# Performance work log

Hardware: AMD Instinct MI355X
Metric: run time of the kernel (lower is better)

Reference implementation:

```python
import jax, jax.numpy as jnp
import numpy as np

N_USERS, N_ITEMS, EMB_DIM = 100000, 50000, 64
NNZ = 4800000
N_LAYERS = 3
KEEP_PROB = 0.5
N_NODES = N_USERS + N_ITEMS


def setup_inputs() -> dict:
    key = jax.random.key(0)
    k0, k1, k2, k3, k4, k5 = jax.random.split(key, 6)
    # Xavier-uniform-like init for embedding tables
    bound = float(np.sqrt(6.0 / (N_USERS + EMB_DIM)))
    user_w = jax.random.uniform(k0, (N_USERS, EMB_DIM), jnp.float32, -bound, bound)
    bound_i = float(np.sqrt(6.0 / (N_ITEMS + EMB_DIM)))
    item_w = jax.random.uniform(k1, (N_ITEMS, EMB_DIM), jnp.float32, -bound_i, bound_i)
    # coalesced sparse norm_adj as an edge list; values ~ symmetric-normalized weights
    rows = jax.random.randint(k2, (NNZ,), 0, N_NODES, jnp.int32)
    cols = jax.random.randint(k3, (NNZ,), 0, N_NODES, jnp.int32)
    vals = jax.random.uniform(k4, (NNZ,), jnp.float32) / 32.0
    # sparse-dropout keep mask (rand + keep_prob, floored -> Bernoulli(keep_prob))
    mask = jax.random.bernoulli(k5, KEEP_PROB, (NNZ,))
    return {"user_w": user_w, "item_w": item_w, "vals": vals,
            "rows": rows, "cols": cols, "mask": mask}


def reference(user_w, item_w, vals, rows, cols, mask):
    # sparse dropout: dropped edges contribute 0 to SpMM; kept ones scaled 1/keep_prob
    v = jnp.where(mask, vals / KEEP_PROB, jnp.zeros((), vals.dtype))
    emb = jnp.concatenate([user_w, item_w], axis=0)  # [N, D]
    acc = emb  # running sum over layer outputs (== stack+mean)
    for _ in range(N_LAYERS):
        # SpMM: out[r] += v_e * emb[c] for each edge e=(r,c)
        emb = jax.ops.segment_sum(v[:, None] * emb[cols], rows,
                                  num_segments=N_NODES)
        acc = acc + emb
    out = acc / (N_LAYERS + 1)
    return out[:N_USERS], out[N_USERS:]
```

## Files before the change

### kernel.cpp

```cpp
#include <hip/hip_runtime.h>
#include <hip/hip_fp16.h>

#define DIM 64
#define KEEP_INV 2.0f
#define BROWS 256
#define NB_MAX 640
#define CAP 5120
#define CHUNK 4096
#define SC_T 512
#define EPT 8
#define COLMASK 0x3FFFF

__global__ void init_kernel(const float4* __restrict__ uw,
                            const float4* __restrict__ iw,
                            uint2* __restrict__ embT0,
                            int n_user_v, int total_v,
                            const unsigned char* __restrict__ mask,
                            int* __restrict__ flag,
                            int* __restrict__ gbcur, int nb) {
    if (blockIdx.x == gridDim.x - 1) {
        __shared__ int cnt;
        if (threadIdx.x == 0) cnt = 0;
        __syncthreads();
        int c = 0;
        for (int i = threadIdx.x; i < 4096; i += blockDim.x)
            c += (mask[i] != 0) ? 1 : 0;
        atomicAdd(&cnt, c);
        __syncthreads();
        if (threadIdx.x == 0) *flag = (cnt * 16 > 4096 * 5) ? 1 : 4;
        for (int i = threadIdx.x; i < nb; i += blockDim.x)
            gbcur[i] = i * CAP;
        return;
    }
    int i = blockIdx.x * blockDim.x + threadIdx.x;
    int gs = (gridDim.x - 1) * blockDim.x;
    for (; i < total_v; i += gs) {
        float4 v = (i < n_user_v) ? uw[i] : iw[i - n_user_v];
        __half2 h0 = __float22half2_rn(make_float2(v.x, v.y));
        __half2 h1 = __float22half2_rn(make_float2(v.z, v.w));
        uint2 pk;
        pk.x = *(unsigned int*)&h0;
        pk.y = *(unsigned int*)&h1;
        embT0[i] = pk;
    }
}

__device__ inline int load_keep8(const unsigned char* mask, int e0, int sm) {
    int keep = 0;
    if (sm == 1) {
        uint2 mv = *(const uint2*)(mask + e0);
#pragma unroll
        for (int j = 0; j < 4; ++j) {
            if ((mv.x >> (8 * j)) & 0xFF) keep |= 1 << j;
            if ((mv.y >> (8 * j)) & 0xFF) keep |= 1 << (4 + j);
        }
    } else {
        const int4* mp = (const int4*)((const int*)mask + e0);
        int4 m0 = mp[0], m1 = mp[1];
        if (m0.x) keep |= 1;  if (m0.y) keep |= 2;
        if (m0.z) keep |= 4;  if (m0.w) keep |= 8;
        if (m1.x) keep |= 16; if (m1.y) keep |= 32;
        if (m1.z) keep |= 64; if (m1.w) keep |= 128;
    }
    return keep;
}

__global__ void __launch_bounds__(SC_T, 8) bucket_scatter_kernel(
        const int* __restrict__ rows, const int* __restrict__ cols,
        const float* __restrict__ vals, const unsigned char* __restrict__ mask,
        const int* __restrict__ flag, int nnz, int nb,
        int* __restrict__ gbcur, int2* __restrict__ X) {
    __shared__ int lhist[NB_MAX];
    __shared__ int lcur[NB_MAX];
    int t = threadIdx.x;
    for (int i = t; i < nb; i += SC_T) lhist[i] = 0;
    __syncthreads();
    int sm = *flag;
    int e0 = blockIdx.x * CHUNK + t * EPT;

    int r[EPT], c[EPT];
    float v[EPT];
    int keep = 0;
    if (e0 + EPT <= nnz) {
        const int4* rp = (const int4*)(rows + e0);
        int4 a0 = rp[0], a1 = rp[1];
        r[0] = a0.x; r[1] = a0.y; r[2] = a0.z; r[3] = a0.w;
        r[4] = a1.x; r[5] = a1.y; r[6] = a1.z; r[7] = a1.w;
        const int4* cp = (const int4*)(cols + e0);
        int4 b0 = cp[0], b1 = cp[1];
        c[0] = b0.x; c[1] = b0.y; c[2] = b0.z; c[3] = b0.w;
        c[4] = b1.x; c[5] = b1.y; c[6] = b1.z; c[7] = b1.w;
        const float4* vp = (const float4*)(vals + e0);
        float4 f0 = vp[0], f1 = vp[1];
        v[0] = f0.x; v[1] = f0.y; v[2] = f0.z; v[3] = f0.w;
        v[4] = f1.x; v[5] = f1.y; v[6] = f1.z; v[7] = f1.w;
        keep = load_keep8(mask, e0, sm);
    } else {
        for (int j = 0; j < EPT; ++j) {
            int idx = e0 + j;
            if (idx < nnz) {
                r[j] = rows[idx];
                c[j] = cols[idx];
                v[j] = vals[idx];
                if (mask[(size_t)idx * sm]) keep |= 1 << j;
            }
        }
    }

#pragma unroll
    for (int j = 0; j < EPT; ++j)
        if ((keep >> j) & 1) atomicAdd(&lhist[r[j] >> 8], 1);
    __syncthreads();
    for (int i = t; i < nb; i += SC_T) {
        int cc = lhist[i];
        lcur[i] = cc ? atomicAdd(&gbcur[i], cc) : 0;
    }
    __syncthreads();
#pragma unroll
    for (int j = 0; j < EPT; ++j) {
        if ((keep >> j) & 1) {
            int b = r[j] >> 8;
            int p = atomicAdd(&lcur[b], 1);
            if (p < (b + 1) * CAP) {
                int2 e;
                e.x = (c[j] & COLMASK) | ((r[j] & 255) << 18);
                e.y = __float_as_int(v[j] * KEEP_INV);
                X[p] = e;
            }
        }
    }
}

__global__ void __launch_bounds__(256) bucket_sort_kernel(
        const int2* __restrict__ X, const int* __restrict__ gbcur, int n_nodes,
        int2* __restrict__ Y, int2* __restrict__ rowse) {
    __shared__ int cnt[BROWS];
    __shared__ int sc[2][BROWS];
    __shared__ int rcur[BROWS];
    int b = blockIdx.x;
    int t = threadIdx.x;
    int s0 = b * CAP;
    int count = min(gbcur[b] - s0, CAP);
    int s1 = s0 + count;
    cnt[t] = 0;
    __syncthreads();
    for (int i = s0 + t; i < s1; i += 256) atomicAdd(&cnt[X[i].x >> 18], 1);
    __syncthreads();
    sc[0][t] = cnt[t];
    __syncthreads();
    int src = 0;
    for (int off = 1; off < BROWS; off <<= 1) {
        sc[src ^ 1][t] = sc[src][t] + ((t >= off) ? sc[src][t - off] : 0);
        __syncthreads();
        src ^= 1;
    }
    int excl = (t == 0) ? 0 : sc[src][t - 1];
    rcur[t] = excl;
    int gr = b * BROWS + t;
    if (gr < n_nodes) {
        int2 se;
        se.x = s0 + excl;
        se.y = s0 + excl + cnt[t];
        rowse[gr] = se;
    }
    __syncthreads();
    for (int i = s0 + t; i < s1; i += 256) {
        int2 e = X[i];
        int ro = e.x >> 18;
        int p = atomicAdd(&rcur[ro], 1);
        int2 o;
        o.x = e.x & COLMASK;
        o.y = e.y;
        Y[s0 + p] = o;
    }
}

template <bool STORE_EMB, bool FINAL>
__global__ void __launch_bounds__(256) spmm_kernel(
        const int2* __restrict__ rowse,
        const int2* __restrict__ edges,
        const uint2* __restrict__ embv16,
        uint2* __restrict__ embB16,
        const uint2* __restrict__ e0tab,
        const uint2* __restrict__ e1tab,
        float4* __restrict__ out,
        int nrows) {
    int wid = blockIdx.x * (blockDim.x >> 6) + (threadIdx.x >> 6);
    if (wid >= nrows) return;
    int lane = threadIdx.x & 63;
    int grp = lane >> 4;
    int l16 = lane & 15;
    int2 se = rowse[wid];
    int start = se.x;
    int end = se.y;

    float4 acc;
    acc.x = acc.y = acc.z = acc.w = 0.f;

    for (int e0 = start; e0 < end; e0 += 16) {
        int c[4];
        float v[4];
#pragma unroll
        for (int k = 0; k < 4; ++k) {
            int idx = e0 + grp + 4 * k;
            int cl = idx < end ? idx : end - 1;
            int2 p = edges[cl];
            c[k] = p.x;
            v[k] = (idx < end) ? __int_as_float(p.y) : 0.f;
        }
        uint2 g[4];
#pragma unroll
        for (int k = 0; k < 4; ++k)
            g[k] = embv16[(size_t)c[k] * 16 + l16];
#pragma unroll
        for (int k = 0; k < 4; ++k) {
            float2 f01 = __half22float2(*(const __half2*)&g[k].x);
            float2 f23 = __half22float2(*(const __half2*)&g[k].y);
            acc.x += v[k] * f01.x;
            acc.y += v[k] * f01.y;
            acc.z += v[k] * f23.x;
            acc.w += v[k] * f23.y;
        }
    }

#pragma unroll
    for (int off = 16; off < 64; off <<= 1) {
        acc.x += __shfl_xor(acc.x, off, 64);
        acc.y += __shfl_xor(acc.y, off, 64);
        acc.z += __shfl_xor(acc.z, off, 64);
        acc.w += __shfl_xor(acc.w, off, 64);
    }

    if (grp == 0) {
        size_t o = (size_t)wid * 16 + l16;
        if (STORE_EMB) {
            __half2 h0 = __float22half2_rn(make_float2(acc.x, acc.y));
            __half2 h1 = __float22half2_rn(make_float2(acc.z, acc.w));
            uint2 pk;
            pk.x = *(unsigned int*)&h0;
            pk.y = *(unsigned int*)&h1;
            embB16[o] = pk;
        }
        if (FINAL) {
            uint2 a = e0tab[o];
            uint2 b = e1tab[o];
            uint2 d = embv16[o];
            float2 a01 = __half22float2(*(const __half2*)&a.x);
            float2 a23 = __half22float2(*(const __half2*)&a.y);
            float2 b01 = __half22float2(*(const __half2*)&b.x);
            float2 b23 = __half22float2(*(const __half2*)&b.y);
            float2 d01 = __half22float2(*(const __half2*)&d.x);
            float2 d23 = __half22float2(*(const __half2*)&d.y);
            float4 ov;
            ov.x = 0.25f * (a01.x + b01.x + d01.x + acc.x);
            ov.y = 0.25f * (a01.y + b01.y + d01.y + acc.y);
            ov.z = 0.25f * (a23.x + b23.x + d23.x + acc.z);
            ov.w = 0.25f * (a23.y + b23.y + d23.y + acc.w);
            out[o] = ov;
        }
    }
}

extern "C" void kernel_launch(void* const* d_in, const int* in_sizes, int n_in,
                              void* d_out, int out_size, void* d_ws, size_t ws_size,
                              hipStream_t stream) {
    const float* user_w = (const float*)d_in[0];
    const float* item_w = (const float*)d_in[1];
    const float* vals   = (const float*)d_in[2];
    const int*   rows   = (const int*)d_in[3];
    const int*   cols   = (const int*)d_in[4];
    const unsigned char* mask = (const unsigned char*)d_in[5];

    const int n_user = in_sizes[0] / DIM;
    const int n_item = in_sizes[1] / DIM;
    const int nnz    = in_sizes[2];
    const int n_nodes = n_user + n_item;
    const int n_elems = n_nodes * DIM;
    const int nb = (n_nodes + BROWS - 1) / BROWS;

    char* ws = (char*)d_ws;
    size_t off = 0;
    auto alloc = [&](size_t bytes) {
        void* p = ws + off;
        off = (off + bytes + 255) & ~(size_t)255;
        return p;
    };
    int*   gbcur  = (int*)alloc((size_t)NB_MAX * 4);
    int*   flag   = (int*)alloc(256);
    int2*  rowse  = (int2*)alloc((size_t)n_nodes * 8);
    int2*  X      = (int2*)alloc((size_t)nb * CAP * 8);
    int2*  Y      = (int2*)alloc((size_t)nb * CAP * 8);
    uint2* embT0  = (uint2*)alloc((size_t)n_nodes * 16 * 8);
    uint2* embT1  = (uint2*)alloc((size_t)n_nodes * 16 * 8);
    uint2* embT2  = (uint2*)X;
    float* outf   = (float*)d_out;

    {
        int total_v = n_elems / 4;
        init_kernel<<<2049, 256, 0, stream>>>((const float4*)user_w,
                                              (const float4*)item_w,
                                              embT0, n_user * DIM / 4, total_v,
                                              mask, flag, gbcur, nb);
    }

    int nchunks = (nnz + CHUNK - 1) / CHUNK;
    bucket_scatter_kernel<<<nchunks, SC_T, 0, stream>>>(rows, cols, vals, mask,
                                                        flag, nnz, nb, gbcur, X);
    bucket_sort_kernel<<<nb, BROWS, 0, stream>>>(X, gbcur, n_nodes, Y, rowse);

    {
        int blocks = (n_nodes + 3) / 4;
        spmm_kernel<true, false><<<blocks, 256, 0, stream>>>(
            rowse, Y, embT0, embT1, embT0, embT1, (float4*)outf, n_nodes);
        spmm_kernel<true, false><<<blocks, 256, 0, stream>>>(
            rowse, Y, embT1, embT2, embT0, embT1, (float4*)outf, n_nodes);
        spmm_kernel<false, true><<<blocks, 256, 0, stream>>>(
            rowse, Y, embT2, embT2, embT0, embT1, (float4*)outf, n_nodes);
    }
}
```

Measured before the change: 266.7 us.

## Pack edges into 32-bit words with truncated half values; stage buckets in LDS

```diff
diff --git a/kernel.cpp b/kernel.cpp
--- a/kernel.cpp
+++ b/kernel.cpp
@@ -133,7 +133,8 @@
 
 __global__ void __launch_bounds__(256) bucket_sort_kernel(
         const int2* __restrict__ X, const int* __restrict__ gbcur, int n_nodes,
-        int2* __restrict__ Y, int2* __restrict__ rowse) {
+        unsigned int* __restrict__ Y, int2* __restrict__ rowse) {
+    __shared__ int2 lbuf[CAP];
     __shared__ int cnt[BROWS];
     __shared__ int sc[2][BROWS];
     __shared__ int rcur[BROWS];
@@ -141,10 +142,13 @@
     int t = threadIdx.x;
     int s0 = b * CAP;
     int count = min(gbcur[b] - s0, CAP);
-    int s1 = s0 + count;
     cnt[t] = 0;
     __syncthreads();
-    for (int i = s0 + t; i < s1; i += 256) atomicAdd(&cnt[X[i].x >> 18], 1);
+    for (int i = t; i < count; i += 256) {
+        int2 e = X[s0 + i];
+        lbuf[i] = e;
+        atomicAdd(&cnt[e.x >> 18], 1);
+    }
     __syncthreads();
     sc[0][t] = cnt[t];
     __syncthreads();
@@ -164,21 +168,22 @@
         rowse[gr] = se;
     }
     __syncthreads();
-    for (int i = s0 + t; i < s1; i += 256) {
-        int2 e = X[i];
+    for (int i = t; i < count; i += 256) {
+        int2 e = lbuf[i];
         int ro = e.x >> 18;
         int p = atomicAdd(&rcur[ro], 1);
-        int2 o;
-        o.x = e.x & COLMASK;
-        o.y = e.y;
-        Y[s0 + p] = o;
+        float vf = __int_as_float(e.y);
+        __half h = __float2half(vf);
+        unsigned int hb = (unsigned int)(*(unsigned short*)&h);
+        unsigned int code = (hb >> 1) & 0x3FFFu;
+        Y[s0 + p] = (code << 18) | (unsigned int)(e.x & COLMASK);
     }
 }
 
 template <bool STORE_EMB, bool FINAL>
 __global__ void __launch_bounds__(256) spmm_kernel(
         const int2* __restrict__ rowse,
-        const int2* __restrict__ edges,
+        const unsigned int* __restrict__ edges,
         const uint2* __restrict__ embv16,
         uint2* __restrict__ embB16,
         const uint2* __restrict__ e0tab,
@@ -204,9 +209,11 @@
         for (int k = 0; k < 4; ++k) {
             int idx = e0 + grp + 4 * k;
             int cl = idx < end ? idx : end - 1;
-            int2 p = edges[cl];
-            c[k] = p.x;
-            v[k] = (idx < end) ? __int_as_float(p.y) : 0.f;
+            unsigned int p = edges[cl];
+            c[k] = (int)(p & COLMASK);
+            unsigned short hb = (unsigned short)((p >> 18) << 1);
+            __half h = *(__half*)&hb;
+            v[k] = (idx < end) ? __half2float(h) : 0.f;
         }
         uint2 g[4];
 #pragma unroll
@@ -289,7 +296,7 @@
     int*   flag   = (int*)alloc(256);
     int2*  rowse  = (int2*)alloc((size_t)n_nodes * 8);
     int2*  X      = (int2*)alloc((size_t)nb * CAP * 8);
-    int2*  Y      = (int2*)alloc((size_t)nb * CAP * 8);
+    unsigned int* Y = (unsigned int*)alloc((size_t)nb * CAP * 4);
     uint2* embT0  = (uint2*)alloc((size_t)n_nodes * 16 * 8);
     uint2* embT1  = (uint2*)alloc((size_t)n_nodes * 16 * 8);
     uint2* embT2  = (uint2*)X;
```

New measurement: 240.9 us. 9.7% less time.
